# Optimization experiments

Hardware: AMD Instinct MI355X
Metric: run time of the kernel (lower is better)

The kernel has to match this reference:

```python
import jax, jax.numpy as jnp
import numpy as np

EMBED_DIM = 1024
NUM_HEADS = 16
HEAD_DIM = EMBED_DIM // NUM_HEADS  # 64
GRID_H, GRID_W = 24, 24
BASE = 10000.0


def rope2d_cache(head_dim=HEAD_DIM, grid_h=GRID_H, grid_w=GRID_W, base=BASE):
    # "Concatenated Embeddings" 2D RoPE cache -> (cos, sin), each [grid_h*grid_w, head_dim]
    pos_dim = head_dim // 2
    inv_freq = 1.0 / (base ** (jnp.arange(0, pos_dim, 2, dtype=jnp.float32) / pos_dim))
    max_grid = max(grid_h, grid_w)
    positions = jnp.arange(max_grid, dtype=jnp.float32)
    freqs = positions[:, None] * inv_freq[None, :]            # [max_grid, pos_dim//2]
    emb_1d = jnp.concatenate([freqs, freqs], axis=-1)          # [max_grid, pos_dim]
    h_emb = jnp.broadcast_to(emb_1d[:grid_h, None, :], (grid_h, grid_w, pos_dim))
    w_emb = jnp.broadcast_to(emb_1d[None, :grid_w, :], (grid_h, grid_w, pos_dim))
    emb_2d = jnp.concatenate([h_emb, w_emb], axis=-1).reshape(-1, head_dim)
    return jnp.cos(emb_2d), jnp.sin(emb_2d)


def rotate_half(x):
    x1, x2 = jnp.split(x, 2, axis=-1)
    return jnp.concatenate([-x2, x1], axis=-1)


def setup_inputs() -> dict:
    key = jax.random.key(0)
    ks = jax.random.split(key, 9)
    B, S, E = 16, GRID_H * GRID_W + 1, EMBED_DIM
    s = 1.0 / np.sqrt(E)
    inp = {
        "hidden_states": jax.random.normal(ks[0], (B, S, E), dtype=jnp.float32),
        "Wq": jax.random.normal(ks[1], (E, E), dtype=jnp.float32) * s,
        "bq": jnp.zeros((E,), dtype=jnp.float32),
        "Wk": jax.random.normal(ks[2], (E, E), dtype=jnp.float32) * s,
        "bk": jnp.zeros((E,), dtype=jnp.float32),
        "Wv": jax.random.normal(ks[3], (E, E), dtype=jnp.float32) * s,
        "bv": jnp.zeros((E,), dtype=jnp.float32),
        "Wo": jax.random.normal(ks[4], (E, E), dtype=jnp.float32) * s,
        "bo": jnp.zeros((E,), dtype=jnp.float32),
    }
    return inp


def reference(hidden_states, Wq, bq, Wk, bk, Wv, bv, Wo, bo):
    B, S, E = hidden_states.shape
    H, D = NUM_HEADS, HEAD_DIM
    scale = D ** -0.5

    def proj(W, b):
        # torch Linear: x @ W.T + b; reshape to [B, H, S, D]
        y = jnp.einsum('bse,fe->bsf', hidden_states, W) + b
        return y.reshape(B, S, H, D).transpose(0, 2, 1, 3)

    q = proj(Wq, bq)
    k = proj(Wk, bk)
    v = proj(Wv, bv)

    cos, sin = rope2d_cache()                 # [num_patches, D]
    cos = cos[None, None, :, :]
    sin = sin[None, None, :, :]

    # CLS token at position 0 is untouched; RoPE applied to patch tokens 1:
    qp = q[:, :, 1:, :]
    kp = k[:, :, 1:, :]
    qp = qp * cos + rotate_half(qp) * sin
    kp = kp * cos + rotate_half(kp) * sin
    q = jnp.concatenate([q[:, :, :1, :], qp], axis=2)
    k = jnp.concatenate([k[:, :, :1, :], kp], axis=2)

    scores = jnp.einsum('bhqd,bhkd->bhqk', q, k) * scale   # [B,H,S,S]
    attn = jax.nn.softmax(scores, axis=-1)
    out = jnp.einsum('bhqk,bhkd->bhqd', attn, v)           # [B,H,S,D]
    out = out.transpose(0, 2, 1, 3).reshape(B, S, E)
    out = jnp.einsum('bse,fe->bsf', out, Wo) + bo
    return out
```

## Files before the change

### kernel.cpp

```cpp
#include <hip/hip_runtime.h>
#include <hip/hip_bf16.h>
#include <stdint.h>

typedef __bf16 bf16_t;
typedef __attribute__((ext_vector_type(4))) float floatx4;
typedef __attribute__((ext_vector_type(8))) __bf16 bf16x8;
typedef __attribute__((ext_vector_type(4))) __bf16 bf16x4;

#define MFMA16(a, b, c) __builtin_amdgcn_mfma_f32_16x16x32_bf16(a, b, c, 0, 0, 0)

#define GLOAD_LDS16(gsrc, ldst)                                                          \
  __builtin_amdgcn_global_load_lds((const __attribute__((address_space(1))) void*)(gsrc),\
                                   (__attribute__((address_space(3))) void*)(ldst),      \
                                   16, 0, 0)

#define BATCH 16
#define SEQ   577
#define EMB   1024
#define NH    16
#define HD    64
#define SPAD  640
#define MROWS (BATCH * SEQ)
#define MPAD  9344

#define EXP_C 0.1803368801111404f

#define OFF_H  0ULL
#define OFF_WQ 19136512ULL
#define OFF_WK 21233664ULL
#define OFF_WV 23330816ULL
#define OFF_WO 25427968ULL
#define OFF_Q  27525120ULL
#define OFF_K  48496640ULL
#define OFF_VT 69468160ULL
#define OFF_AO 90439680ULL

__global__ __launch_bounds__(256) void k_cast(
    const float4* __restrict__ hs, const float4* __restrict__ wq,
    const float4* __restrict__ wk, const float4* __restrict__ wv,
    const float4* __restrict__ wo, bf16x4* __restrict__ hb, bf16x4* __restrict__ wqb,
    bf16x4* __restrict__ wkb, bf16x4* __restrict__ wvb, bf16x4* __restrict__ wob) {
  int idx = blockIdx.x * 256 + threadIdx.x;
  const int H4 = MROWS * EMB / 4;
  const int W4 = EMB * EMB / 4;
  const float4* src;
  bf16x4* dst;
  int i;
  if (idx < H4) {
    src = hs; dst = hb; i = idx;
  } else {
    int r = idx - H4;
    int w = r / W4;
    if (w >= 4) return;
    i = r - w * W4;
    src = (w == 0) ? wq : (w == 1) ? wk : (w == 2) ? wv : wo;
    dst = (w == 0) ? wqb : (w == 1) ? wkb : (w == 2) ? wvb : wob;
  }
  float4 v = src[i];
  bf16x4 o;
  o.x = (bf16_t)v.x; o.y = (bf16_t)v.y; o.z = (bf16_t)v.z; o.w = (bf16_t)v.w;
  dst[i] = o;
}

__global__ __launch_bounds__(256, 3) void k_qkv(const bf16_t* __restrict__ A,
                                                const bf16_t* __restrict__ Wq,
                                                const bf16_t* __restrict__ Wk,
                                                const bf16_t* __restrict__ Wv,
                                                const float* __restrict__ bq,
                                                const float* __restrict__ bk,
                                                const float* __restrict__ bv,
                                                bf16_t* __restrict__ qb,
                                                bf16_t* __restrict__ kb,
                                                bf16_t* __restrict__ vtb) {
  __shared__ __align__(16) bf16_t smem[2 * 10240];
  const int hh = blockIdx.x;
  const int n0 = hh * 64;
  const int m0 = blockIdx.y * 128;
  const int t = threadIdx.x;
  const int wid = t >> 6, lane = t & 63, quad = lane >> 4, c = lane & 15;

  const int srow0 = t >> 2;
  const int srow1 = 64 + srow0;
  const int soff = (((t & 3) ^ ((t >> 3) & 3)) * 8);

#define QKV_STAGE(buf, k0)                                                                  \
  {                                                                                         \
    bf16_t* As_ = smem + (buf) * 10240;                                                     \
    bf16_t* Bs_ = As_ + 4096;                                                               \
    GLOAD_LDS16(A + (size_t)(m0 + srow0) * EMB + (k0) + soff, (char*)As_ + (wid * 64) * 16);\
    GLOAD_LDS16(A + (size_t)(m0 + srow1) * EMB + (k0) + soff,                               \
                (char*)As_ + (256 + wid * 64) * 16);                                        \
    GLOAD_LDS16(Wq + (size_t)(n0 + srow0) * EMB + (k0) + soff, (char*)Bs_ + (wid * 64) * 16);\
    GLOAD_LDS16(Wk + (size_t)(n0 + srow0) * EMB + (k0) + soff,                              \
                (char*)Bs_ + 4096 + (wid * 64) * 16);                                       \
    GLOAD_LDS16(Wv + (size_t)(n0 + srow0) * EMB + (k0) + soff,                              \
                (char*)Bs_ + 8192 + (wid * 64) * 16);                                       \
  }

  floatx4 acc[3][2][4];
#pragma unroll
  for (int z = 0; z < 3; z++)
#pragma unroll
    for (int i = 0; i < 2; i++)
#pragma unroll
      for (int j = 0; j < 4; j++) {
        floatx4 zz = {0.f, 0.f, 0.f, 0.f};
        acc[z][i][j] = zz;
      }

  QKV_STAGE(0, 0);
  __syncthreads();
  int cur = 0;
  for (int kt = 0; kt < 32; kt++) {
    if (kt < 31) QKV_STAGE(cur ^ 1, (kt + 1) * 32);
    const bf16_t* Asc = smem + cur * 10240;
    const bf16_t* Bsc = Asc + 4096;
    bf16x8 af[2];
#pragma unroll
    for (int mi = 0; mi < 2; mi++) {
      int row = wid * 32 + mi * 16 + c;
      af[mi] = *(const bf16x8*)(Asc + row * 32 + (quad * 8 ^ (((row >> 1) & 3) << 3)));
    }
#pragma unroll
    for (int z = 0; z < 3; z++) {
      bf16x8 bfr[4];
#pragma unroll
      for (int ni = 0; ni < 4; ni++) {
        int row = ni * 16 + c;
        bfr[ni] = *(const bf16x8*)(Bsc + z * 2048 + row * 32 + (quad * 8 ^ (((row >> 1) & 3) << 3)));
      }
#pragma unroll
      for (int mi = 0; mi < 2; mi++)
#pragma unroll
        for (int ni = 0; ni < 4; ni++) acc[z][mi][ni] = MFMA16(af[mi], bfr[ni], acc[z][mi][ni]);
    }
    __syncthreads();
    cur ^= 1;
  }
#undef QKV_STAGE

  const float invf = exp2f(-(float)c * 0.8304820237218405f);

  for (int z = 0; z < 3; z++) {
    const float* bias = (z == 0) ? bq : (z == 1) ? bk : bv;
    float bias_v[4];
#pragma unroll
    for (int ni = 0; ni < 4; ni++) bias_v[ni] = bias[n0 + ni * 16 + c];
#pragma unroll
    for (int mi = 0; mi < 2; mi++) {
#pragma unroll
      for (int r = 0; r < 4; r++) {
        int m = m0 + wid * 32 + mi * 16 + quad * 4 + r;
        if (m >= MROWS) continue;
        int bb = m / SEQ;
        int s = m - bb * SEQ;
        if (z < 2) {
          float ch = 1.f, sh = 0.f, cw = 1.f, sw = 0.f;
          if (s > 0) {
            int p = s - 1;
            int hp = p / 24, wp2 = p - (p / 24) * 24;
            __sincosf((float)hp * invf, &sh, &ch);
            __sincosf((float)wp2 * invf, &sw, &cw);
          }
          bf16_t* dst = (z == 0) ? qb : kb;
          size_t rowoff = ((size_t)(bb * NH + hh) * SPAD + s) * HD;
#pragma unroll
          for (int ni = 0; ni < 4; ni++) {
            float val = acc[z][mi][ni][r] + bias_v[ni];
            float part = acc[z][mi][ni ^ 2][r] + bias_v[ni ^ 2];
            float rot = (ni < 2) ? -part : part;
            float cs = (ni < 2) ? ch : cw;
            float sn = (ni < 2) ? sh : sw;
            dst[rowoff + ni * 16 + c] = (bf16_t)(val * cs + rot * sn);
          }
        } else {
          size_t base = (size_t)(bb * NH + hh) * HD;
#pragma unroll
          for (int ni = 0; ni < 4; ni++) {
            float val = acc[z][mi][ni][r] + bias_v[ni];
            int d = ni * 16 + c;
            vtb[(base + d) * SPAD + s] = (bf16_t)val;
          }
        }
      }
    }
  }
}

#define PSTR 72
#define OSTR 66
#define MI   3
__global__ __launch_bounds__(256, 3) void k_attn(const bf16_t* __restrict__ qb,
                                                 const bf16_t* __restrict__ kb,
                                                 const bf16_t* __restrict__ vtb,
                                                 bf16_t* __restrict__ ao) {
  __shared__ __align__(16) bf16_t smem[13824];
  bf16_t* Ks = smem;
  bf16_t* Vs = smem + 4608;
  bf16_t* Ps = smem + 9216;
  const int t = threadIdx.x, wid = t >> 6, lane = t & 63, quad = lane >> 4, c = lane & 15;
  const int hh = blockIdx.x, bb = blockIdx.y, qt = blockIdx.z;
  const size_t bh = (size_t)bb * NH + hh;
  const bf16_t* qall = qb + bh * SPAD * HD;
  const bf16_t* qbase = qall + (size_t)qt * 192 * HD;
  const bf16_t* kbase = kb + bh * SPAD * HD;
  const bf16_t* vbase = vtb + bh * HD * SPAD;
  bf16_t* Pw = Ps + wid * 1152;

  bf16x8 aq[MI][2];
#pragma unroll
  for (int mi = 0; mi < MI; mi++)
#pragma unroll
    for (int h = 0; h < 2; h++)
      aq[mi][h] = *(const bf16x8*)(qbase + (size_t)(wid * 48 + mi * 16 + c) * HD + h * 32 + quad * 8);

  uint4 kr[2], vr[2];
#pragma unroll
  for (int j = 0; j < 2; j++) {
    int ci = j * 256 + t;
    int row = ci >> 3, off = (ci & 7) * 8;
    kr[j] = *(const uint4*)(kbase + (size_t)row * HD + off);
    vr[j] = *(const uint4*)(vbase + (size_t)row * SPAD + off);
  }

  floatx4 acc_o[MI][4];
  float lsum[MI][4];
#pragma unroll
  for (int mi = 0; mi < MI; mi++) {
    floatx4 z = {0.f, 0.f, 0.f, 0.f};
#pragma unroll
    for (int nd = 0; nd < 4; nd++) acc_o[mi][nd] = z;
#pragma unroll
    for (int r = 0; r < 4; r++) lsum[mi][r] = 0.f;
  }

  for (int kt = 0; kt < 9; kt++) {
    __syncthreads();
#pragma unroll
    for (int j = 0; j < 2; j++) {
      int ci = j * 256 + t;
      int row = ci >> 3, off = (ci & 7) * 8;
      *(uint4*)((char*)Ks + (row * PSTR + off) * 2) = kr[j];
      *(uint4*)((char*)Vs + (row * PSTR + off) * 2) = vr[j];
    }
    __syncthreads();
    if (kt < 8) {
#pragma unroll
      for (int j = 0; j < 2; j++) {
        int ci = j * 256 + t;
        int row = ci >> 3, off = (ci & 7) * 8;
        kr[j] = *(const uint4*)(kbase + (size_t)((kt + 1) * 64 + row) * HD + off);
        vr[j] = *(const uint4*)(vbase + (size_t)row * SPAD + (kt + 1) * 64 + off);
      }
    }

    floatx4 sc[MI][4];
#pragma unroll
    for (int ni = 0; ni < 4; ni++) {
      bf16x8 k0 = *(const bf16x8*)(Ks + (ni * 16 + c) * PSTR + quad * 8);
      bf16x8 k1 = *(const bf16x8*)(Ks + (ni * 16 + c) * PSTR + 32 + quad * 8);
#pragma unroll
      for (int mi = 0; mi < MI; mi++) {
        floatx4 zz = {0.f, 0.f, 0.f, 0.f};
        zz = MFMA16(aq[mi][0], k0, zz);
        zz = MFMA16(aq[mi][1], k1, zz);
        sc[mi][ni] = zz;
      }
    }

#pragma unroll
    for (int mi = 0; mi < MI; mi++) {
#pragma unroll
      for (int ni = 0; ni < 4; ni++)
#pragma unroll
        for (int r = 0; r < 4; r++) {
          float p = exp2f(sc[mi][ni][r] * EXP_C);
          lsum[mi][r] += p;
          Pw[(quad * 4 + r) * PSTR + ni * 16 + c] = (bf16_t)p;
        }
      bf16x8 pa0 = *(const bf16x8*)(Pw + c * PSTR + quad * 8);
      bf16x8 pa1 = *(const bf16x8*)(Pw + c * PSTR + 32 + quad * 8);
#pragma unroll
      for (int nd = 0; nd < 4; nd++) {
        bf16x8 v0 = *(const bf16x8*)(Vs + (nd * 16 + c) * PSTR + quad * 8);
        bf16x8 v1 = *(const bf16x8*)(Vs + (nd * 16 + c) * PSTR + 32 + quad * 8);
        acc_o[mi][nd] = MFMA16(pa0, v0, acc_o[mi][nd]);
        acc_o[mi][nd] = MFMA16(pa1, v1, acc_o[mi][nd]);
      }
    }
  }

  {
    bf16x8 klast[2];
#pragma unroll
    for (int h = 0; h < 2; h++) {
      bf16x8 kk;
#pragma unroll
      for (int i = 0; i < 8; i++) kk[i] = (bf16_t)0.0f;
      if (c == 0) kk = *(const bf16x8*)(kbase + (size_t)576 * HD + h * 32 + quad * 8);
      klast[h] = kk;
    }
    float vlast[4];
#pragma unroll
    for (int nd = 0; nd < 4; nd++)
      vlast[nd] = (float)vbase[(size_t)(nd * 16 + c) * SPAD + 576];
#pragma unroll
    for (int mi = 0; mi < MI; mi++) {
      floatx4 zz = {0.f, 0.f, 0.f, 0.f};
      zz = MFMA16(aq[mi][0], klast[0], zz);
      zz = MFMA16(aq[mi][1], klast[1], zz);
#pragma unroll
      for (int r = 0; r < 4; r++) {
        float p = exp2f(zz[r] * EXP_C);
        p = __shfl(p, quad * 16, 64);
#pragma unroll
        for (int nd = 0; nd < 4; nd++) acc_o[mi][nd][r] += p * vlast[nd];
        if (c == 0) lsum[mi][r] += p;
      }
    }
  }

#pragma unroll
  for (int mi = 0; mi < MI; mi++)
#pragma unroll
    for (int r = 0; r < 4; r++) {
      float l = lsum[mi][r];
      l += __shfl_xor(l, 1, 64);
      l += __shfl_xor(l, 2, 64);
      l += __shfl_xor(l, 4, 64);
      l += __shfl_xor(l, 8, 64);
      lsum[mi][r] = l;
    }

  {
    const int rsub = lane >> 3, c8 = lane & 7;
#pragma unroll
    for (int mi = 0; mi < MI; mi++) {
#pragma unroll
      for (int r = 0; r < 4; r++) {
        float inv_l = 1.f / lsum[mi][r];
        int row = quad * 4 + r;
#pragma unroll
        for (int nd = 0; nd < 4; nd++)
          Pw[row * OSTR + nd * 16 + c] = (bf16_t)(acc_o[mi][nd][r] * inv_l);
      }
#pragma unroll
      for (int j = 0; j < 2; j++) {
        int row = j * 8 + rsub;
        bf16x8 ov = *(const bf16x8*)(Pw + row * OSTR + c8 * 8);
        int q = qt * 192 + wid * 48 + mi * 16 + row;
        if (q < SEQ) {
          size_t mrow = (size_t)bb * SEQ + q;
          *(bf16x8*)(ao + mrow * EMB + hh * HD + c8 * 8) = ov;
        }
      }
    }
  }

  if (qt == 2) {
    float* Pt = (float*)Ks;
    float* Ot = Pt + 584;
    __syncthreads();
    bf16x8 qv8[8];
    const bf16_t* q576 = qall + (size_t)576 * HD;
#pragma unroll
    for (int ch = 0; ch < 8; ch++) qv8[ch] = *(const bf16x8*)(q576 + ch * 8);
#pragma unroll
    for (int rep = 0; rep < 3; rep++) {
      int j = t + rep * 256;
      if (j < SEQ) {
        const bf16_t* krow = kbase + (size_t)j * HD;
        float s = 0.f;
#pragma unroll
        for (int ch = 0; ch < 8; ch++) {
          bf16x8 kx = *(const bf16x8*)(krow + ch * 8);
#pragma unroll
          for (int e = 0; e < 8; e++) s += (float)qv8[ch][e] * (float)kx[e];
        }
        Pt[j] = exp2f(s * EXP_C);
      }
    }
    __syncthreads();
    {
      int d = t & 63, g = t >> 6;
      int j0 = g * 145, j1 = (g == 3) ? SEQ : (j0 + 145);
      const bf16_t* vrow = vbase + (size_t)d * SPAD;
      float o = 0.f;
      for (int j = j0; j < j1; j++) o += Pt[j] * (float)vrow[j];
      Ot[g * 64 + d] = o;
    }
    __syncthreads();
    if (wid == 0) {
      float l = 0.f;
      for (int k2 = lane; k2 < SEQ; k2 += 64) l += Pt[k2];
#pragma unroll
      for (int off = 1; off < 64; off <<= 1) l += __shfl_xor(l, off, 64);
      float sum = Ot[lane] + Ot[64 + lane] + Ot[128 + lane] + Ot[192 + lane];
      ao[((size_t)bb * SEQ + 576) * EMB + hh * HD + lane] = (bf16_t)(sum / l);
    }
  }
}

__global__ __launch_bounds__(256) void k_oproj(const bf16_t* __restrict__ A,
                                               const bf16_t* __restrict__ Wo,
                                               const float* __restrict__ bo,
                                               float* __restrict__ out) {
  __shared__ __align__(16) bf16_t smem[2 * 8192];
  const int n0 = blockIdx.x * 128, m0 = blockIdx.y * 128;
  const int t = threadIdx.x;
  const int wid = t >> 6, lane = t & 63, quad = lane >> 4, c = lane & 15;
  const int wr = wid >> 1, wc = wid & 1;
  const int srow0 = t >> 2;
  const int srow1 = 64 + srow0;
  const int soff = (((t & 3) ^ ((t >> 3) & 3)) * 8);

#define OPROJ_STAGE(buf, k0)                                                                 \
  {                                                                                          \
    bf16_t* As_ = smem + (buf) * 8192;                                                       \
    bf16_t* Bs_ = As_ + 4096;                                                                \
    GLOAD_LDS16(A + (size_t)(m0 + srow0) * EMB + (k0) + soff, (char*)As_ + (wid * 64) * 16); \
    GLOAD_LDS16(A + (size_t)(m0 + srow1) * EMB + (k0) + soff,                                \
                (char*)As_ + (256 + wid * 64) * 16);                                         \
    GLOAD_LDS16(Wo + (size_t)(n0 + srow0) * EMB + (k0) + soff, (char*)Bs_ + (wid * 64) * 16);\
    GLOAD_LDS16(Wo + (size_t)(n0 + srow1) * EMB + (k0) + soff,                               \
                (char*)Bs_ + (256 + wid * 64) * 16);                                         \
  }

  floatx4 acc[4][4];
#pragma unroll
  for (int i = 0; i < 4; i++)
#pragma unroll
    for (int j = 0; j < 4; j++) {
      floatx4 z = {0.f, 0.f, 0.f, 0.f};
      acc[i][j] = z;
    }

  OPROJ_STAGE(0, 0);
  __syncthreads();
  int cur = 0;
  for (int kt = 0; kt < 32; kt++) {
    if (kt < 31) OPROJ_STAGE(cur ^ 1, (kt + 1) * 32);
    const bf16_t* Asc = smem + cur * 8192;
    const bf16_t* Bsc = Asc + 4096;
    bf16x8 af[4], bfr[4];
#pragma unroll
    for (int mi = 0; mi < 4; mi++) {
      int row = wr * 64 + mi * 16 + c;
      af[mi] = *(const bf16x8*)(Asc + row * 32 + (quad * 8 ^ (((row >> 1) & 3) << 3)));
    }
#pragma unroll
    for (int ni = 0; ni < 4; ni++) {
      int row = wc * 64 + ni * 16 + c;
      bfr[ni] = *(const bf16x8*)(Bsc + row * 32 + (quad * 8 ^ (((row >> 1) & 3) << 3)));
    }
#pragma unroll
    for (int mi = 0; mi < 4; mi++)
#pragma unroll
      for (int ni = 0; ni < 4; ni++) acc[mi][ni] = MFMA16(af[mi], bfr[ni], acc[mi][ni]);
    __syncthreads();
    cur ^= 1;
  }
#undef OPROJ_STAGE

  float bias_v[4];
#pragma unroll
  for (int ni = 0; ni < 4; ni++) bias_v[ni] = bo[n0 + wc * 64 + ni * 16 + c];
#pragma unroll
  for (int mi = 0; mi < 4; mi++)
#pragma unroll
    for (int r = 0; r < 4; r++) {
      int m = m0 + wr * 64 + mi * 16 + quad * 4 + r;
      if (m >= MROWS) continue;
#pragma unroll
      for (int ni = 0; ni < 4; ni++)
        out[(size_t)m * EMB + n0 + wc * 64 + ni * 16 + c] = acc[mi][ni][r] + bias_v[ni];
    }
}

extern "C" void kernel_launch(void* const* d_in, const int* in_sizes, int n_in, void* d_out,
                              int out_size, void* d_ws, size_t ws_size, hipStream_t stream) {
  const float* hs = (const float*)d_in[0];
  const float* Wq = (const float*)d_in[1];
  const float* bq = (const float*)d_in[2];
  const float* Wk = (const float*)d_in[3];
  const float* bk = (const float*)d_in[4];
  const float* Wv = (const float*)d_in[5];
  const float* bv = (const float*)d_in[6];
  const float* Wo = (const float*)d_in[7];
  const float* bo = (const float*)d_in[8];
  float* out = (float*)d_out;
  char* ws = (char*)d_ws;

  bf16_t* hb = (bf16_t*)(ws + OFF_H);
  bf16_t* wqb = (bf16_t*)(ws + OFF_WQ);
  bf16_t* wkb = (bf16_t*)(ws + OFF_WK);
  bf16_t* wvb = (bf16_t*)(ws + OFF_WV);
  bf16_t* wob = (bf16_t*)(ws + OFF_WO);
  bf16_t* qbuf = (bf16_t*)(ws + OFF_Q);
  bf16_t* kbuf = (bf16_t*)(ws + OFF_K);
  bf16_t* vtbuf = (bf16_t*)(ws + OFF_VT);
  bf16_t* aob = (bf16_t*)(ws + OFF_AO);


  k_cast<<<13328, 256, 0, stream>>>((const float4*)hs, (const float4*)Wq, (const float4*)Wk,
                                    (const float4*)Wv, (const float4*)Wo, (bf16x4*)hb,
                                    (bf16x4*)wqb, (bf16x4*)wkb, (bf16x4*)wvb, (bf16x4*)wob);

  dim3 gq(16, 73);
  k_qkv<<<gq, 256, 0, stream>>>(hb, wqb, wkb, wvb, bq, bk, bv, qbuf, kbuf, vtbuf);

  dim3 ga(16, 16, 3);
  k_attn<<<ga, 256, 0, stream>>>(qbuf, kbuf, vtbuf, aob);

  dim3 go(8, 73);
  k_oproj<<<go, 256, 0, stream>>>(aob, wob, bo, out);
}
```

Before: 312.8 us.

## Double-buffer K/V tiles in LDS to halve per-iteration barriers

The attention kernel now keeps two LDS buffers for the K and V tiles. It writes the next tile into the alternate buffer while computing on the current one, and prefetches two tiles ahead in registers. This replaces two __syncthreads per key tile with one and is meant to overlap LDS stores and global loads with the MFMA work. It raises LDS use from about 27KB to 45KB per block, which with launch_bounds(256,3) may reduce how many blocks fit per CU. It also adds an unused srow/ssoff variable.

Result: slower. 403.4 us (+29.0%).

```diff
diff --git a/kernel.cpp b/kernel.cpp
--- a/kernel.cpp
+++ b/kernel.cpp
@@ -194,10 +194,8 @@
                                                  const bf16_t* __restrict__ kb,
                                                  const bf16_t* __restrict__ vtb,
                                                  bf16_t* __restrict__ ao) {
-  __shared__ __align__(16) bf16_t smem[13824];
-  bf16_t* Ks = smem;
-  bf16_t* Vs = smem + 4608;
-  bf16_t* Ps = smem + 9216;
+  __shared__ __align__(16) bf16_t smem[23040];
+  bf16_t* Ps = smem + 18432;
   const int t = threadIdx.x, wid = t >> 6, lane = t & 63, quad = lane >> 4, c = lane & 15;
   const int hh = blockIdx.x, bb = blockIdx.y, qt = blockIdx.z;
   const size_t bh = (size_t)bb * NH + hh;
@@ -214,6 +212,8 @@
     for (int h = 0; h < 2; h++)
       aq[mi][h] = *(const bf16x8*)(qbase + (size_t)(wid * 48 + mi * 16 + c) * HD + h * 32 + quad * 8);
 
+  const int srow = (t * 2) >> 3, ssoff = ((t * 2) & 7) * 8;
+
   uint4 kr[2], vr[2];
 #pragma unroll
   for (int j = 0; j < 2; j++) {
@@ -222,6 +222,21 @@
     kr[j] = *(const uint4*)(kbase + (size_t)row * HD + off);
     vr[j] = *(const uint4*)(vbase + (size_t)row * SPAD + off);
   }
+#pragma unroll
+  for (int j = 0; j < 2; j++) {
+    int ci = j * 256 + t;
+    int row = ci >> 3, off = (ci & 7) * 8;
+    *(uint4*)((char*)(smem) + (row * PSTR + off) * 2) = kr[j];
+    *(uint4*)((char*)(smem + 9216) + (row * PSTR + off) * 2) = vr[j];
+  }
+#pragma unroll
+  for (int j = 0; j < 2; j++) {
+    int ci = j * 256 + t;
+    int row = ci >> 3, off = (ci & 7) * 8;
+    kr[j] = *(const uint4*)(kbase + (size_t)(64 + row) * HD + off);
+    vr[j] = *(const uint4*)(vbase + (size_t)row * SPAD + 64 + off);
+  }
+  __syncthreads();
 
   floatx4 acc_o[MI][4];
   float lsum[MI][4];
@@ -234,31 +249,36 @@
     for (int r = 0; r < 4; r++) lsum[mi][r] = 0.f;
   }
 
+  int cur = 0;
   for (int kt = 0; kt < 9; kt++) {
-    __syncthreads();
-#pragma unroll
-    for (int j = 0; j < 2; j++) {
-      int ci = j * 256 + t;
-      int row = ci >> 3, off = (ci & 7) * 8;
-      *(uint4*)((char*)Ks + (row * PSTR + off) * 2) = kr[j];
-      *(uint4*)((char*)Vs + (row * PSTR + off) * 2) = vr[j];
-    }
-    __syncthreads();
+    const bf16_t* Ksc = smem + cur * 4608;
+    const bf16_t* Vsc = smem + 9216 + cur * 4608;
     if (kt < 8) {
+      bf16_t* Ksn = smem + (cur ^ 1) * 4608;
+      bf16_t* Vsn = smem + 9216 + (cur ^ 1) * 4608;
 #pragma unroll
       for (int j = 0; j < 2; j++) {
         int ci = j * 256 + t;
         int row = ci >> 3, off = (ci & 7) * 8;
-        kr[j] = *(const uint4*)(kbase + (size_t)((kt + 1) * 64 + row) * HD + off);
-        vr[j] = *(const uint4*)(vbase + (size_t)row * SPAD + (kt + 1) * 64 + off);
+        *(uint4*)((char*)Ksn + (row * PSTR + off) * 2) = kr[j];
+        *(uint4*)((char*)Vsn + (row * PSTR + off) * 2) = vr[j];
+      }
+    }
+    if (kt < 7) {
+#pragma unroll
+      for (int j = 0; j < 2; j++) {
+        int ci = j * 256 + t;
+        int row = ci >> 3, off = (ci & 7) * 8;
+        kr[j] = *(const uint4*)(kbase + (size_t)((kt + 2) * 64 + row) * HD + off);
+        vr[j] = *(const uint4*)(vbase + (size_t)row * SPAD + (kt + 2) * 64 + off);
       }
     }
 
     floatx4 sc[MI][4];
 #pragma unroll
     for (int ni = 0; ni < 4; ni++) {
-      bf16x8 k0 = *(const bf16x8*)(Ks + (ni * 16 + c) * PSTR + quad * 8);
-      bf16x8 k1 = *(const bf16x8*)(Ks + (ni * 16 + c) * PSTR + 32 + quad * 8);
+      bf16x8 k0 = *(const bf16x8*)(Ksc + (ni * 16 + c) * PSTR + quad * 8);
+      bf16x8 k1 = *(const bf16x8*)(Ksc + (ni * 16 + c) * PSTR + 32 + quad * 8);
 #pragma unroll
       for (int mi = 0; mi < MI; mi++) {
         floatx4 zz = {0.f, 0.f, 0.f, 0.f};
@@ -282,12 +302,15 @@
       bf16x8 pa1 = *(const bf16x8*)(Pw + c * PSTR + 32 + quad * 8);
 #pragma unroll
       for (int nd = 0; nd < 4; nd++) {
-        bf16x8 v0 = *(const bf16x8*)(Vs + (nd * 16 + c) * PSTR + quad * 8);
-        bf16x8 v1 = *(const bf16x8*)(Vs + (nd * 16 + c) * PSTR + 32 + quad * 8);
+        bf16x8 v0 = *(const bf16x8*)(Vsc + (nd * 16 + c) * PSTR + quad * 8);
+        bf16x8 v1 = *(const bf16x8*)(Vsc + (nd * 16 + c) * PSTR + 32 + quad * 8);
         acc_o[mi][nd] = MFMA16(pa0, v0, acc_o[mi][nd]);
         acc_o[mi][nd] = MFMA16(pa1, v1, acc_o[mi][nd]);
       }
     }
+
+    __syncthreads();
+    cur ^= 1;
   }
 
   {
@@ -358,7 +381,7 @@
   }
 
   if (qt == 2) {
-    float* Pt = (float*)Ks;
+    float* Pt = (float*)smem;
     float* Ot = Pt + 584;
     __syncthreads();
     bf16x8 qv8[8];
```
